# Performance work log

Hardware: AMD Instinct MI355X
Metric: run time of the kernel (lower is better)

Reference implementation:

```python
import jax, jax.numpy as jnp
import numpy as np

LN_EPS = 1e-5
MASK_FILL = -1e10


def setup_inputs() -> dict:
    key = jax.random.key(0)
    ks = jax.random.split(key, 6)
    b, lq, lk, d = 8, 2048, 2048, 256
    q = jax.random.normal(ks[0], (b, lq, d), dtype=jnp.float32)
    k = jax.random.normal(ks[1], (b, lk, d), dtype=jnp.float32)
    v = jax.random.normal(ks[2], (b, lk, d), dtype=jnp.float32)
    # additive-score weight, scaled so logits are O(1)
    shared_attn = jax.random.normal(ks[3], (1, 2 * d), dtype=jnp.float32) / jnp.sqrt(jnp.float32(2 * d))
    fc_w = jax.random.normal(ks[4], (d, d), dtype=jnp.float32) / jnp.sqrt(jnp.float32(d))
    ln_gamma = jnp.ones((d,), dtype=jnp.float32)
    ln_beta = jnp.zeros((d,), dtype=jnp.float32)
    mask = jax.random.randint(ks[5], (b, lq, lk), 0, 2).astype(bool)
    return {"q": q, "k": k, "v": v, "shared_attn": shared_attn,
            "fc_w": fc_w, "ln_gamma": ln_gamma, "ln_beta": ln_beta, "mask": mask}


def reference(q, k, v, shared_attn, fc_w, ln_gamma, ln_beta, mask):
    d_k = q.shape[-1]
    residual = q
    # F.linear(cat([q_exp, k_exp], -1), W) with W:(1, 2*d_k) decomposes as
    # score[b,i,j] = q[b,i] . w_q + k[b,j] . w_k  (rank-1 additive score)
    w_q = shared_attn[0, :d_k]
    w_k = shared_attn[0, d_k:]
    sq = jnp.einsum('bid,d->bi', q, w_q)          # (b, lq)
    sk = jnp.einsum('bjd,d->bj', k, w_k)          # (b, lk)
    attn = sq[:, :, None] + sk[:, None, :]        # (b, lq, lk)
    attn = jnp.where(mask, jnp.float32(MASK_FILL), attn)
    attn = jax.nn.softmax(attn, axis=2)
    out = jnp.einsum('bij,bjd->bid', attn, v)     # (b, lq, d_v)
    out = out @ fc_w.T                            # F.linear(out, fc_w)
    x = out + residual
    mu = jnp.mean(x, axis=-1, keepdims=True)
    var = jnp.var(x, axis=-1, keepdims=True)
    out = (x - mu) / jnp.sqrt(var + LN_EPS) * ln_gamma + ln_beta
    return (out, attn)
```

## Files before the change

### kernel.cpp

```cpp
#include <hip/hip_runtime.h>
#include <hip/hip_bf16.h>

#define BB 8
#define LQ 2048
#define LK 2048
#define DD 256
#define OUT0_N (BB*LQ*DD)

typedef short s16x8 __attribute__((ext_vector_type(8)));
typedef float f32x4 __attribute__((ext_vector_type(4)));

__device__ __forceinline__ unsigned short f2b(float x){
  unsigned int u = __float_as_uint(x);
  u += 0x7fffu + ((u >> 16) & 1u);
  return (unsigned short)(u >> 16);
}
__device__ __forceinline__ float b2f(unsigned short h){
  return __uint_as_float(((unsigned int)h) << 16);
}
__device__ __forceinline__ float ldf(const void* p, long i, int bf){
  return bf ? b2f(((const unsigned short*)p)[i]) : ((const float*)p)[i];
}
__device__ __forceinline__ s16x8 ld8(const void* p, long i, int bf){
  if (bf) return *(const s16x8*)((const unsigned short*)p + i);
  const float* f = (const float*)p + i;
  float4 a = *(const float4*)(f);
  float4 c = *(const float4*)(f + 4);
  s16x8 r;
  r[0]=(short)f2b(a.x); r[1]=(short)f2b(a.y); r[2]=(short)f2b(a.z); r[3]=(short)f2b(a.w);
  r[4]=(short)f2b(c.x); r[5]=(short)f2b(c.y); r[6]=(short)f2b(c.z); r[7]=(short)f2b(c.w);
  return r;
}
__device__ __forceinline__ float wsum(float v){
  #pragma unroll
  for (int o=32;o;o>>=1) v += __shfl_xor(v, o, 64);
  return v;
}

__device__ __forceinline__ void detect_flags(const void* q, const void* mask,
                                             int& mbytes, int& bf){
  __shared__ int s_bf, s_mb;
  int t = threadIdx.x;
  if (t == 0){ s_bf = 0; s_mb = 0; }
  __syncthreads();
  if (t < 256){
    float x = fabsf(((const float*)q)[t]);
    if (x > 1e-6f && x < 100.0f) atomicAdd(&s_bf, 1);
    unsigned int mw = ((const unsigned int*)mask)[t];
    if (mw > 1u) atomicOr(&s_mb, 1);
  }
  __syncthreads();
  bf = (s_bf < 128) ? 1 : 0;
  mbytes = s_mb;
}

__global__ __launch_bounds__(256) void k_prep(const void* q, const void* kk,
    const void* v, const void* sh, const void* fc, const void* mask,
    float* e, unsigned short* vtf){
  int mbytes, bf;
  detect_flags(q, mask, mbytes, bf);
  (void)mbytes;
  int lane = threadIdx.x & 63;

  if (blockIdx.x >= 1024){
    int wid = ((blockIdx.x - 1024) << 2) + (threadIdx.x >> 6);
    long base = (long)wid * DD + lane * 4;
    float acc;
    if (bf){
      ushort4 kv = *(const ushort4*)((const unsigned short*)kk + base);
      ushort4 wv = *(const ushort4*)((const unsigned short*)sh + DD + lane*4);
      acc = b2f(kv.x)*b2f(wv.x) + b2f(kv.y)*b2f(wv.y)
          + b2f(kv.z)*b2f(wv.z) + b2f(kv.w)*b2f(wv.w);
    } else {
      float4 kv = *(const float4*)((const float*)kk + base);
      float4 wv = *(const float4*)((const float*)sh + DD + lane*4);
      acc = kv.x*wv.x + kv.y*wv.y + kv.z*wv.z + kv.w*wv.w;
    }
    acc = wsum(acc);
    if (lane == 0) e[wid] = __expf(acc);
    return;
  }

  int wid  = (blockIdx.x << 2) + (threadIdx.x >> 6);
  int dbase = (wid & 15) << 4;
  int jbase = (wid >> 4) << 6;
  int r = lane & 15, g = lane >> 4;
  f32x4 acc[4];
  #pragma unroll
  for (int t2=0;t2<4;t2++) acc[t2] = (f32x4){0.f,0.f,0.f,0.f};
  #pragma unroll
  for (int ks = 0; ks < 8; ++ks){
    int k0 = ks*32 + g*8;
    s16x8 bv = ld8(fc, (long)(dbase + r)*DD + k0, bf);
    #pragma unroll
    for (int t2 = 0; t2 < 4; ++t2){
      s16x8 a = ld8(v, (long)(jbase + t2*16 + r)*DD + k0, bf);
      acc[t2] = __builtin_amdgcn_mfma_f32_16x16x32_bf16(a, bv, acc[t2], 0, 0, 0);
    }
  }
  int b  = jbase >> 11;
  int jj = jbase & 2047;
  int d  = dbase + r;
  #pragma unroll
  for (int t2 = 0; t2 < 4; ++t2){
    int kidx = (jj >> 3) + t2*2 + (g >> 1);
    long idx = ((long)(b*256 + kidx))*2048 + (long)d*8 + (g & 1)*4;
    ushort4 w4;
    w4.x = f2b(acc[t2][0]); w4.y = f2b(acc[t2][1]);
    w4.z = f2b(acc[t2][2]); w4.w = f2b(acc[t2][3]);
    *(ushort4*)(vtf + idx) = w4;
  }
}

__global__ __launch_bounds__(256) void k_pack(const void* q, const void* mask,
    const float* e, void* d_out, unsigned int* bits, float* scale){
  int mbytes, bf;
  detect_flags(q, mask, mbytes, bf);
  int row  = (blockIdx.x << 2) + (threadIdx.x >> 6);
  int lane = threadIdx.x & 63;
  int b = row >> 11;
  const float* eb = e + b * LK;
  long rowm = (long)row * LK;
  unsigned int bw = 0;
  float4 ev[8];
  float s = 0.f;
  #pragma unroll
  for (int w = 0; w < 8; ++w){
    int j = (w << 8) + (lane << 2);
    unsigned int m4;
    if (mbytes){
      unsigned int mb = *(const unsigned int*)((const unsigned char*)mask + rowm + j);
      m4 = (mb & 1u) | ((mb >> 7) & 2u) | ((mb >> 14) & 4u) | ((mb >> 21) & 8u);
    } else {
      int4 mi = *(const int4*)((const int*)mask + rowm + j);
      m4 = (mi.x?1u:0u) | (mi.y?2u:0u) | (mi.z?4u:0u) | (mi.w?8u:0u);
    }
    bw |= m4 << (w*4);
    ev[w] = *(const float4*)(eb + j);
    if (!(m4 & 1u)) s += ev[w].x;
    if (!(m4 & 2u)) s += ev[w].y;
    if (!(m4 & 4u)) s += ev[w].z;
    if (!(m4 & 8u)) s += ev[w].w;
  }
  s = wsum(s);
  float scal = (s > 0.f) ? (1.0f/s) : -1.0f;
  bits[(long)row*64 + lane] = bw;
  if (lane == 0) scale[row] = scal;
  #pragma unroll
  for (int w = 0; w < 8; ++w){
    int j = (w << 8) + (lane << 2);
    float p0,p1,p2,p3;
    if (scal < 0.f){ p0=p1=p2=p3 = 1.0f/2048.0f; }
    else {
      p0 = (bw >> (w*4  )) & 1u ? 0.f : ev[w].x * scal;
      p1 = (bw >> (w*4+1)) & 1u ? 0.f : ev[w].y * scal;
      p2 = (bw >> (w*4+2)) & 1u ? 0.f : ev[w].z * scal;
      p3 = (bw >> (w*4+3)) & 1u ? 0.f : ev[w].w * scal;
    }
    if (bf){
      ushort4 u4; u4.x=f2b(p0); u4.y=f2b(p1); u4.z=f2b(p2); u4.w=f2b(p3);
      *(ushort4*)((unsigned short*)d_out + OUT0_N + rowm + j) = u4;
    } else {
      float4 f4 = {p0,p1,p2,p3};
      *(float4*)((float*)d_out + OUT0_N + rowm + j) = f4;
    }
  }
}

__device__ __forceinline__ s16x8 afrag(const unsigned int (*bits_s)[66],
    const unsigned short* e16_s, int row, int kk){
  int w0 = (kk >> 2) & 63;
  int nib4 = (kk >> 8) << 2;
  unsigned lo = (bits_s[row][w0]   >> nib4) & 0xFu;
  unsigned hi = (bits_s[row][w0+1] >> nib4) & 0xFu;
  unsigned m8 = lo | (hi << 4);
  union { s16x8 v; unsigned u[4]; } a;
  a.v = *(const s16x8*)(&e16_s[kk]);
  #pragma unroll
  for (int i = 0; i < 4; ++i){
    unsigned w = a.u[i];
    w = (m8 & (1u << (2*i)))   ? (w & 0xFFFF0000u) : w;
    w = (m8 & (1u << (2*i+1))) ? (w & 0x0000FFFFu) : w;
    a.u[i] = w;
  }
  return a.v;
}

__global__ __launch_bounds__(512, 4) void k_pvf(void* d_out, const unsigned short* vtf,
    const void* q, const void* gamp, const void* betp, const void* mask,
    const unsigned int* bits, const float* e, const float* scaleg){
  __shared__ unsigned int bits_s[32][66];
  __shared__ __align__(16) unsigned short e16_s[LK];
  __shared__ __align__(16) float red[2][32][132];
  __shared__ float scale_s[32];
  __shared__ float gs[256], bs[256];
  int mbytes, bf;
  detect_flags(q, mask, mbytes, bf);
  (void)mbytes;
  int o     = ((blockIdx.x & 7) << 6) + (blockIdx.x >> 3);
  int b     = o >> 6;
  int rbase = (o & 63) << 5;
  int t = threadIdx.x, lane = t & 63, wid = t >> 6;
  int nh = wid & 1, ks = wid >> 1;
  int r16 = lane >> 4, c16 = lane & 15;
  int dbase = nh << 7;

  { float4 ef = ((const float4*)(e + b*LK))[t];
    ushort4 u; u.x=f2b(ef.x); u.y=f2b(ef.y); u.z=f2b(ef.z); u.w=f2b(ef.w);
    *(ushort4*)(&e16_s[t*4]) = u; }
  { int rr = t >> 4, wq = (t & 15) << 2;
    uint4 wv = *(const uint4*)(bits + ((long)(b*LQ + rbase + rr))*64 + wq);
    bits_s[rr][wq+0]=wv.x; bits_s[rr][wq+1]=wv.y;
    bits_s[rr][wq+2]=wv.z; bits_s[rr][wq+3]=wv.w; }
  if (t < 32) scale_s[t] = scaleg[(long)b*LQ + rbase + t];
  if (t < 256){ gs[t] = ldf(gamp, t, bf); bs[t] = ldf(betp, t, bf); }
  __syncthreads();

  float sc0 = scale_s[c16];
  float sc1 = scale_s[16 + c16];
  s16x8 cf;
  #pragma unroll
  for (int i = 0; i < 8; ++i) cf[i] = (short)0x3A00;

  const unsigned short* vtfb = vtf + (long)b * 256 * 2048;
  f32x4 acc[2][8];
  #pragma unroll
  for (int i=0;i<2;i++)
    #pragma unroll
    for (int j=0;j<8;j++) acc[i][j] = (f32x4){0.f,0.f,0.f,0.f};

  for (int s = 0; s < 16; ++s){
    int k0 = (ks << 9) + (s << 5);
    const unsigned short* bp = vtfb + ((long)((k0 >> 3) + r16)*256 + dbase + c16)*8;
    s16x8 A0 = (sc0 < 0.f) ? cf : afrag(bits_s, e16_s, c16,      k0 + r16*8);
    s16x8 A1 = (sc1 < 0.f) ? cf : afrag(bits_s, e16_s, 16 + c16, k0 + r16*8);
    {
      s16x8 B0 = *(const s16x8*)(bp);
      s16x8 B1 = *(const s16x8*)(bp + 128);
      s16x8 B2 = *(const s16x8*)(bp + 256);
      s16x8 B3 = *(const s16x8*)(bp + 384);
      acc[0][0] = __builtin_amdgcn_mfma_f32_16x16x32_bf16(A0, B0, acc[0][0], 0,0,0);
      acc[1][0] = __builtin_amdgcn_mfma_f32_16x16x32_bf16(A1, B0, acc[1][0], 0,0,0);
      acc[0][1] = __builtin_amdgcn_mfma_f32_16x16x32_bf16(A0, B1, acc[0][1], 0,0,0);
      acc[1][1] = __builtin_amdgcn_mfma_f32_16x16x32_bf16(A1, B1, acc[1][1], 0,0,0);
      acc[0][2] = __builtin_amdgcn_mfma_f32_16x16x32_bf16(A0, B2, acc[0][2], 0,0,0);
      acc[1][2] = __builtin_amdgcn_mfma_f32_16x16x32_bf16(A1, B2, acc[1][2], 0,0,0);
      acc[0][3] = __builtin_amdgcn_mfma_f32_16x16x32_bf16(A0, B3, acc[0][3], 0,0,0);
      acc[1][3] = __builtin_amdgcn_mfma_f32_16x16x32_bf16(A1, B3, acc[1][3], 0,0,0);
    }
    {
      s16x8 B4 = *(const s16x8*)(bp + 512);
      s16x8 B5 = *(const s16x8*)(bp + 640);
      s16x8 B6 = *(const s16x8*)(bp + 768);
      s16x8 B7 = *(const s16x8*)(bp + 896);
      acc[0][4] = __builtin_amdgcn_mfma_f32_16x16x32_bf16(A0, B4, acc[0][4], 0,0,0);
      acc[1][4] = __builtin_amdgcn_mfma_f32_16x16x32_bf16(A1, B4, acc[1][4], 0,0,0);
      acc[0][5] = __builtin_amdgcn_mfma_f32_16x16x32_bf16(A0, B5, acc[0][5], 0,0,0);
      acc[1][5] = __builtin_amdgcn_mfma_f32_16x16x32_bf16(A1, B5, acc[1][5], 0,0,0);
      acc[0][6] = __builtin_amdgcn_mfma_f32_16x16x32_bf16(A0, B6, acc[0][6], 0,0,0);
      acc[1][6] = __builtin_amdgcn_mfma_f32_16x16x32_bf16(A1, B6, acc[1][6], 0,0,0);
      acc[0][7] = __builtin_amdgcn_mfma_f32_16x16x32_bf16(A0, B7, acc[0][7], 0,0,0);
      acc[1][7] = __builtin_amdgcn_mfma_f32_16x16x32_bf16(A1, B7, acc[1][7], 0,0,0);
    }
  }

  #pragma unroll
  for (int r = 1; r < 4; ++r){
    if (ks == r){
      #pragma unroll
      for (int mi = 0; mi < 2; ++mi)
        #pragma unroll
        for (int ni = 0; ni < 8; ++ni)
          #pragma unroll
          for (int reg = 0; reg < 4; ++reg)
            red[nh][mi*16 + r16*4 + reg][ni*16 + c16] = acc[mi][ni][reg];
    }
    __syncthreads();
    if (ks == 0){
      #pragma unroll
      for (int mi = 0; mi < 2; ++mi)
        #pragma unroll
        for (int ni = 0; ni < 8; ++ni)
          #pragma unroll
          for (int reg = 0; reg < 4; ++reg)
            acc[mi][ni][reg] += red[nh][mi*16 + r16*4 + reg][ni*16 + c16];
    }
    __syncthreads();
  }
  if (ks == 0){
    #pragma unroll
    for (int mi = 0; mi < 2; ++mi)
      #pragma unroll
      for (int ni = 0; ni < 8; ++ni)
        #pragma unroll
        for (int reg = 0; reg < 4; ++reg)
          red[nh][mi*16 + r16*4 + reg][ni*16 + c16] = acc[mi][ni][reg];
  }
  __syncthreads();

  {
    int row = t >> 4, cg = t & 15;
    int nh2 = cg >> 3, coff = (cg & 7) << 4;
    float sc = scale_s[row];
    float sce = (sc < 0.f) ? 1.0f : sc;
    long grow = (long)b*LQ + rbase + row;
    float xv[16];
    float ps = 0.f, pq = 0.f;
    #pragma unroll
    for (int i4 = 0; i4 < 4; ++i4){
      float4 rv = *(const float4*)(&red[nh2][row][coff + i4*4]);
      float rr[4] = {rv.x, rv.y, rv.z, rv.w};
      int col0 = (cg << 4) + i4*4;
      float qv[4];
      if (bf){
        ushort4 qu = *(const ushort4*)((const unsigned short*)q + grow*DD + col0);
        qv[0]=b2f(qu.x); qv[1]=b2f(qu.y); qv[2]=b2f(qu.z); qv[3]=b2f(qu.w);
      } else {
        float4 qf = *(const float4*)((const float*)q + grow*DD + col0);
        qv[0]=qf.x; qv[1]=qf.y; qv[2]=qf.z; qv[3]=qf.w;
      }
      #pragma unroll
      for (int i = 0; i < 4; ++i){
        float x = rr[i]*sce + qv[i];
        xv[i4*4 + i] = x;
        ps += x; pq += x*x;
      }
    }
    ps += __shfl_xor(ps, 1, 64); pq += __shfl_xor(pq, 1, 64);
    ps += __shfl_xor(ps, 2, 64); pq += __shfl_xor(pq, 2, 64);
    ps += __shfl_xor(ps, 4, 64); pq += __shfl_xor(pq, 4, 64);
    ps += __shfl_xor(ps, 8, 64); pq += __shfl_xor(pq, 8, 64);
    float mu = ps * (1.0f/256.0f);
    float var = pq * (1.0f/256.0f) - mu*mu;
    float rs = rsqrtf(var + 1e-5f);
    #pragma unroll
    for (int i4 = 0; i4 < 4; ++i4){
      int col0 = (cg << 4) + i4*4;
      float y[4];
      #pragma unroll
      for (int i = 0; i < 4; ++i){
        int col = col0 + i;
        y[i] = (xv[i4*4 + i] - mu) * rs * gs[col] + bs[col];
      }
      long oi = grow*(long)DD + col0;
      if (bf){
        ushort4 u4; u4.x=f2b(y[0]); u4.y=f2b(y[1]); u4.z=f2b(y[2]); u4.w=f2b(y[3]);
        *(ushort4*)((unsigned short*)d_out + oi) = u4;
      } else {
        float4 f4 = {y[0],y[1],y[2],y[3]};
        *(float4*)((float*)d_out + oi) = f4;
      }
    }
  }
}

extern "C" void kernel_launch(void* const* d_in, const int* in_sizes, int n_in,
                              void* d_out, int out_size, void* d_ws, size_t ws_size,
                              hipStream_t stream) {
  const void* q    = d_in[0];
  const void* k    = d_in[1];
  const void* v    = d_in[2];
  const void* sh   = d_in[3];
  const void* fc   = d_in[4];
  const void* gam  = d_in[5];
  const void* bet  = d_in[6];
  const void* mask = d_in[7];

  float*          e      = (float*)((char*)d_ws + 65536);
  float*          scale  = (float*)((char*)d_ws + 131072);
  unsigned int*   bits   = (unsigned int*)((char*)d_ws + 262144);
  unsigned short* vtf    = (unsigned short*)((char*)d_ws + 4456448);

  k_prep<<<5120, 256, 0, stream>>>(q, k, v, sh, fc, mask, e, vtf);
  k_pack<<<4096, 256, 0, stream>>>(q, mask, e, d_out, bits, scale);
  k_pvf <<<512,  512, 0, stream>>>(d_out, vtf, q, gam, bet, mask, bits, e, scale);
}
```

Before: 145.6 us.

## Fuse mask packing and attention-probability writeout into the PV/LayerNorm kernel

Removes the separate k_pack kernel and has each k_pvf block compute mask bits, row softmax scales and write the attention matrix for its own 32 rows directly into shared memory. This drops one kernel launch and the global round trip for the bits and scale buffers. In exchange, the large attention-matrix write and mask read now happen inside the PV kernel prologue, before any MFMA work, in a grid of only 512 blocks. That may serialize memory traffic with compute and cut the parallelism available for that bandwidth-heavy phase.

```diff
diff --git a/kernel.cpp b/kernel.cpp
--- a/kernel.cpp
+++ b/kernel.cpp
@@ -112,61 +112,6 @@
   }
 }
 
-__global__ __launch_bounds__(256) void k_pack(const void* q, const void* mask,
-    const float* e, void* d_out, unsigned int* bits, float* scale){
-  int mbytes, bf;
-  detect_flags(q, mask, mbytes, bf);
-  int row  = (blockIdx.x << 2) + (threadIdx.x >> 6);
-  int lane = threadIdx.x & 63;
-  int b = row >> 11;
-  const float* eb = e + b * LK;
-  long rowm = (long)row * LK;
-  unsigned int bw = 0;
-  float4 ev[8];
-  float s = 0.f;
-  #pragma unroll
-  for (int w = 0; w < 8; ++w){
-    int j = (w << 8) + (lane << 2);
-    unsigned int m4;
-    if (mbytes){
-      unsigned int mb = *(const unsigned int*)((const unsigned char*)mask + rowm + j);
-      m4 = (mb & 1u) | ((mb >> 7) & 2u) | ((mb >> 14) & 4u) | ((mb >> 21) & 8u);
-    } else {
-      int4 mi = *(const int4*)((const int*)mask + rowm + j);
-      m4 = (mi.x?1u:0u) | (mi.y?2u:0u) | (mi.z?4u:0u) | (mi.w?8u:0u);
-    }
-    bw |= m4 << (w*4);
-    ev[w] = *(const float4*)(eb + j);
-    if (!(m4 & 1u)) s += ev[w].x;
-    if (!(m4 & 2u)) s += ev[w].y;
-    if (!(m4 & 4u)) s += ev[w].z;
-    if (!(m4 & 8u)) s += ev[w].w;
-  }
-  s = wsum(s);
-  float scal = (s > 0.f) ? (1.0f/s) : -1.0f;
-  bits[(long)row*64 + lane] = bw;
-  if (lane == 0) scale[row] = scal;
-  #pragma unroll
-  for (int w = 0; w < 8; ++w){
-    int j = (w << 8) + (lane << 2);
-    float p0,p1,p2,p3;
-    if (scal < 0.f){ p0=p1=p2=p3 = 1.0f/2048.0f; }
-    else {
-      p0 = (bw >> (w*4  )) & 1u ? 0.f : ev[w].x * scal;
-      p1 = (bw >> (w*4+1)) & 1u ? 0.f : ev[w].y * scal;
-      p2 = (bw >> (w*4+2)) & 1u ? 0.f : ev[w].z * scal;
-      p3 = (bw >> (w*4+3)) & 1u ? 0.f : ev[w].w * scal;
-    }
-    if (bf){
-      ushort4 u4; u4.x=f2b(p0); u4.y=f2b(p1); u4.z=f2b(p2); u4.w=f2b(p3);
-      *(ushort4*)((unsigned short*)d_out + OUT0_N + rowm + j) = u4;
-    } else {
-      float4 f4 = {p0,p1,p2,p3};
-      *(float4*)((float*)d_out + OUT0_N + rowm + j) = f4;
-    }
-  }
-}
-
 __device__ __forceinline__ s16x8 afrag(const unsigned int (*bits_s)[66],
     const unsigned short* e16_s, int row, int kk){
   int w0 = (kk >> 2) & 63;
@@ -188,7 +133,7 @@
 
 __global__ __launch_bounds__(512, 4) void k_pvf(void* d_out, const unsigned short* vtf,
     const void* q, const void* gamp, const void* betp, const void* mask,
-    const unsigned int* bits, const float* e, const float* scaleg){
+    const float* e){
   __shared__ unsigned int bits_s[32][66];
   __shared__ __align__(16) unsigned short e16_s[LK];
   __shared__ __align__(16) float red[2][32][132];
@@ -196,7 +141,6 @@
   __shared__ float gs[256], bs[256];
   int mbytes, bf;
   detect_flags(q, mask, mbytes, bf);
-  (void)mbytes;
   int o     = ((blockIdx.x & 7) << 6) + (blockIdx.x >> 3);
   int b     = o >> 6;
   int rbase = (o & 63) << 5;
@@ -204,16 +148,64 @@
   int nh = wid & 1, ks = wid >> 1;
   int r16 = lane >> 4, c16 = lane & 15;
   int dbase = nh << 7;
-
-  { float4 ef = ((const float4*)(e + b*LK))[t];
+  const float* eb = e + b * LK;
+
+  { float4 ef = ((const float4*)eb)[t];
     ushort4 u; u.x=f2b(ef.x); u.y=f2b(ef.y); u.z=f2b(ef.z); u.w=f2b(ef.w);
     *(ushort4*)(&e16_s[t*4]) = u; }
-  { int rr = t >> 4, wq = (t & 15) << 2;
-    uint4 wv = *(const uint4*)(bits + ((long)(b*LQ + rbase + rr))*64 + wq);
-    bits_s[rr][wq+0]=wv.x; bits_s[rr][wq+1]=wv.y;
-    bits_s[rr][wq+2]=wv.z; bits_s[rr][wq+3]=wv.w; }
-  if (t < 32) scale_s[t] = scaleg[(long)b*LQ + rbase + t];
   if (t < 256){ gs[t] = ldf(gamp, t, bf); bs[t] = ldf(betp, t, bf); }
+
+  unsigned short* attn16 = (unsigned short*)d_out + OUT0_N;
+  float*          attn32 = (float*)d_out + OUT0_N;
+  #pragma unroll 1
+  for (int rr = 0; rr < 4; ++rr){
+    int row = (wid << 2) + rr;
+    long rowm = ((long)(b*LQ + rbase + row)) * (long)LK;
+    unsigned int bw = 0;
+    float4 ev[8];
+    float s = 0.f;
+    #pragma unroll
+    for (int w = 0; w < 8; ++w){
+      int j = (w << 8) + (lane << 2);
+      unsigned int m4;
+      if (mbytes){
+        unsigned int mb = *(const unsigned int*)((const unsigned char*)mask + rowm + j);
+        m4 = (mb & 1u) | ((mb >> 7) & 2u) | ((mb >> 14) & 4u) | ((mb >> 21) & 8u);
+      } else {
+        int4 mi = *(const int4*)((const int*)mask + rowm + j);
+        m4 = (mi.x?1u:0u) | (mi.y?2u:0u) | (mi.z?4u:0u) | (mi.w?8u:0u);
+      }
+      bw |= m4 << (w*4);
+      ev[w] = *(const float4*)(eb + j);
+      if (!(m4 & 1u)) s += ev[w].x;
+      if (!(m4 & 2u)) s += ev[w].y;
+      if (!(m4 & 4u)) s += ev[w].z;
+      if (!(m4 & 8u)) s += ev[w].w;
+    }
+    s = wsum(s);
+    float scal = (s > 0.f) ? (1.0f/s) : -1.0f;
+    bits_s[row][lane] = bw;
+    if (lane == 0) scale_s[row] = scal;
+    #pragma unroll
+    for (int w = 0; w < 8; ++w){
+      int j = (w << 8) + (lane << 2);
+      float p0,p1,p2,p3;
+      if (scal < 0.f){ p0=p1=p2=p3 = 1.0f/2048.0f; }
+      else {
+        p0 = (bw >> (w*4  )) & 1u ? 0.f : ev[w].x * scal;
+        p1 = (bw >> (w*4+1)) & 1u ? 0.f : ev[w].y * scal;
+        p2 = (bw >> (w*4+2)) & 1u ? 0.f : ev[w].z * scal;
+        p3 = (bw >> (w*4+3)) & 1u ? 0.f : ev[w].w * scal;
+      }
+      if (bf){
+        ushort4 u4; u4.x=f2b(p0); u4.y=f2b(p1); u4.z=f2b(p2); u4.w=f2b(p3);
+        *(ushort4*)(attn16 + rowm + j) = u4;
+      } else {
+        float4 f4 = {p0,p1,p2,p3};
+        *(float4*)(attn32 + rowm + j) = f4;
+      }
+    }
+  }
   __syncthreads();
 
   float sc0 = scale_s[c16];
@@ -366,12 +358,9 @@
   const void* bet  = d_in[6];
   const void* mask = d_in[7];
 
-  float*          e      = (float*)((char*)d_ws + 65536);
-  float*          scale  = (float*)((char*)d_ws + 131072);
-  unsigned int*   bits   = (unsigned int*)((char*)d_ws + 262144);
-  unsigned short* vtf    = (unsigned short*)((char*)d_ws + 4456448);
+  float*          e   = (float*)((char*)d_ws + 65536);
+  unsigned short* vtf = (unsigned short*)((char*)d_ws + 4456448);
 
   k_prep<<<5120, 256, 0, stream>>>(q, k, v, sh, fc, mask, e, vtf);
-  k_pack<<<4096, 256, 0, stream>>>(q, mask, e, d_out, bits, scale);
-  k_pvf <<<512,  512, 0, stream>>>(d_out, vtf, q, gam, bet, mask, bits, e, scale);
-}
+  k_pvf <<<512,  512, 0, stream>>>(d_out, vtf, q, gam, bet, mask, e);
+}
```

Result: faster. 130.3 us (median of 2 runs) (-10.5%).
